# Optimization experiments

Hardware: AMD Instinct MI355X
Metric: run time of the kernel (lower is better)

Reference implementation:

```python
import jax, jax.numpy as jnp
import numpy as np

B, N, D, E, R, V = 8, 256, 64, 64, 32, 64
D_MIN, D_MAX = 0.0, 20.0


def _ln(x, g, b, eps=1e-5):
    m = jnp.mean(x, -1, keepdims=True)
    v = jnp.mean(jnp.square(x - m), -1, keepdims=True)
    return (x - m) * jax.lax.rsqrt(v + eps) * g + b


def setup_inputs() -> dict:
    key = jax.random.key(0)
    ks = jax.random.split(key, 12)
    w = lambda k, s: jax.random.normal(k, s, jnp.float32) * 0.02
    emb = w(ks[0], (V, D)).at[0].set(0.0)  # padding_idx=0 -> zero row
    return {
        "ligand_atom": jax.random.randint(ks[1], (B, N), 0, V),
        "ligand_pos": jax.random.normal(ks[2], (B, N, 3), jnp.float32),
        "edge_mask": jnp.ones((B, N, N), jnp.float32),
        "emb_table": emb,
        "ne_w": w(ks[3], (D, D)), "ne_b": jnp.zeros((D,), jnp.float32),
        "ne_g": jnp.ones((D,), jnp.float32), "ne_beta": jnp.zeros((D,), jnp.float32),
        "ee_w1": w(ks[4], (2 * D + R, E)), "ee_b1": jnp.zeros((E,), jnp.float32),
        "ee_w2": w(ks[5], (E, E)), "ee_b2": jnp.zeros((E,), jnp.float32),
        "ee_w3": w(ks[6], (E, E)), "ee_b3": jnp.zeros((E,), jnp.float32),
        "ee_g": jnp.ones((E,), jnp.float32), "ee_beta": jnp.zeros((E,), jnp.float32),
        "na_w1": w(ks[7], (D + E, D)), "na_b1": jnp.zeros((D,), jnp.float32),
        "na_w2": w(ks[8], (D, D)), "na_b2": jnp.zeros((D,), jnp.float32),
        "na_w3": w(ks[9], (D, D)), "na_b3": jnp.zeros((D,), jnp.float32),
        "na_g": jnp.ones((D,), jnp.float32), "na_beta": jnp.zeros((D,), jnp.float32),
    }


def reference(ligand_atom, ligand_pos, edge_mask, emb_table,
              ne_w, ne_b, ne_g, ne_beta,
              ee_w1, ee_b1, ee_w2, ee_b2, ee_w3, ee_b3, ee_g, ee_beta,
              na_w1, na_b1, na_w2, na_b2, na_w3, na_b3, na_g, na_beta):
    # node_embedder: Embedding -> ReLU -> Linear -> LayerNorm
    node = _ln(jax.nn.relu(emb_table[ligand_atom]) @ ne_w + ne_b, ne_g, ne_beta)  # [B,N,D]

    # pairwise distances, masked
    diff = ligand_pos[:, None, :, :] - ligand_pos[:, :, None, :]
    dist = jnp.sqrt(jnp.sum(diff * diff, -1) + 1e-10) * edge_mask  # [B,N,N]

    # RBF featurization
    mu = jnp.linspace(D_MIN, D_MAX, R)
    sigma = (D_MAX - D_MIN) / R
    rbf = jnp.exp(-jnp.square((dist[..., None] - mu) / sigma)) * edge_mask[..., None]  # [B,N,N,R]

    # edge_embedder: first Linear decomposed over [src | tar | rbf] slices (same math
    # as concat+Linear, avoids materializing the [B,N,N,2D+R] concat)
    Ws, Wt, Wr = ee_w1[:D], ee_w1[D:2 * D], ee_w1[2 * D:]
    # src[b,i,j]=node[b,j] (unsqueeze(1)), tar[b,i,j]=node[b,i] (unsqueeze(2))
    h = jax.nn.relu((node @ Ws)[:, None] + (node @ Wt)[:, :, None]
                    + jnp.einsum('bijr,re->bije', rbf, Wr) + ee_b1)
    h = jax.nn.relu(h @ ee_w2 + ee_b2)
    edge = _ln(h @ ee_w3 + ee_b3, ee_g, ee_beta)  # [B,N,N,E]

    # masked mean over dim=1, gated by (atom type clamped at 1)
    denom = jnp.sum(edge_mask[..., None], axis=1) + 1e-10  # [B,N,1]
    gate = jnp.minimum(ligand_atom, 1).astype(edge.dtype)[..., None]
    agg = jnp.sum(edge, axis=1) / denom * gate  # [B,N,E]

    x = jnp.concatenate([node, agg], -1)
    x = jax.nn.relu(x @ na_w1 + na_b1)
    x = jax.nn.relu(x @ na_w2 + na_b2)
    x = _ln(x @ na_w3 + na_b3, na_g, na_beta)
    return node + x, edge
```

## Files before the change

### kernel.cpp

```cpp
#include <hip/hip_runtime.h>
#include <math.h>

#define NB 8
#define NN 256
#define ND 64
#define NE 64
#define NR 32

typedef _Float16 half8 __attribute__((ext_vector_type(8)));
typedef _Float16 half4 __attribute__((ext_vector_type(4)));
typedef __fp16 fp16x2 __attribute__((ext_vector_type(2)));
typedef float f32x4 __attribute__((ext_vector_type(4)));
typedef int int4v __attribute__((ext_vector_type(4)));

__device__ __forceinline__ float rl(float x, int lane) {
    return __uint_as_float(__builtin_amdgcn_readlane(__float_as_uint(x), lane));
}

__device__ __forceinline__ float wave_sum64(float v) {
#pragma unroll
    for (int m = 32; m >= 1; m >>= 1) v += __shfl_xor(v, m, 64);
    return v;
}

__device__ __forceinline__ half4 mk4(float a, float b, float c, float d) {
    fp16x2 lo = __builtin_amdgcn_cvt_pkrtz(a, b);
    fp16x2 hi = __builtin_amdgcn_cvt_pkrtz(c, d);
    half4 r;
    r[0] = (_Float16)lo[0]; r[1] = (_Float16)lo[1];
    r[2] = (_Float16)hi[0]; r[3] = (_Float16)hi[1];
    return r;
}

__global__ __launch_bounds__(256) void k1_node(
    const int* __restrict__ atom, const float* __restrict__ emb,
    const float* __restrict__ ne_w, const float* __restrict__ ne_b,
    const float* __restrict__ ne_g, const float* __restrict__ ne_beta,
    const float* __restrict__ ee_w1, const float* __restrict__ ee_b1,
    const float* __restrict__ ee_w2, const float* __restrict__ ee_w3,
    float* __restrict__ ws_node, float* __restrict__ ws_s, float* __restrict__ ws_t,
    _Float16* __restrict__ wrT, _Float16* __restrict__ w2tH, _Float16* __restrict__ w3tH)
{
    if (blockIdx.x >= 512) {
        const int tid = (blockIdx.x - 512) * 256 + threadIdx.x;
        for (int idx = tid; idx < NE * NR; idx += 512) {
            const int e = idx >> 5, r = idx & 31;
            wrT[idx] = (_Float16)ee_w1[(2 * ND + r) * NE + e];
        }
        for (int idx = tid; idx < NE * NE; idx += 512) {
            const int n = idx >> 6, k = idx & 63;
            w2tH[idx] = (_Float16)ee_w2[k * NE + n];
            w3tH[idx] = (_Float16)ee_w3[k * NE + n];
        }
        return;
    }

    const int wave = threadIdx.x >> 6;
    const int lane = threadIdx.x & 63;
    const int row  = blockIdx.x * 4 + wave;

    const int a = atom[row];
    float ev = fmaxf(emb[a * ND + lane], 0.f);

    float a0 = 0.f, a1 = 0.f, a2 = 0.f, a3 = 0.f;
#pragma unroll
    for (int k = 0; k < ND; k += 4) {
        a0 = fmaf(rl(ev, k + 0), ne_w[(k + 0) * ND + lane], a0);
        a1 = fmaf(rl(ev, k + 1), ne_w[(k + 1) * ND + lane], a1);
        a2 = fmaf(rl(ev, k + 2), ne_w[(k + 2) * ND + lane], a2);
        a3 = fmaf(rl(ev, k + 3), ne_w[(k + 3) * ND + lane], a3);
    }
    float pre = ne_b[lane] + ((a0 + a1) + (a2 + a3));

    float mean = wave_sum64(pre) * (1.f / 64.f);
    float dv = pre - mean;
    float var = wave_sum64(dv * dv) * (1.f / 64.f);
    float nv = dv * rsqrtf(var + 1e-5f) * ne_g[lane] + ne_beta[lane];
    ws_node[row * ND + lane] = nv;

    float s0 = 0.f, s1 = 0.f, t0 = 0.f, t1 = 0.f;
#pragma unroll
    for (int k = 0; k < ND; k += 2) {
        const float n0 = rl(nv, k), n1 = rl(nv, k + 1);
        s0 = fmaf(n0, ee_w1[(k)     * NE + lane], s0);
        s1 = fmaf(n1, ee_w1[(k + 1) * NE + lane], s1);
        t0 = fmaf(n0, ee_w1[(ND + k)     * NE + lane], t0);
        t1 = fmaf(n1, ee_w1[(ND + k + 1) * NE + lane], t1);
    }
    ws_s[row * NE + lane] = ee_b1[lane] + s0 + s1;
    ws_t[row * NE + lane] = t0 + t1;
}

__global__ __launch_bounds__(256, 4) void k2_edge(
    const float* __restrict__ pos, const float* __restrict__ mask,
    const int* __restrict__ atom,
    const float* __restrict__ ws_s, const float* __restrict__ ws_t,
    const _Float16* __restrict__ wrT,
    const float* __restrict__ ee_b2, const float* __restrict__ ee_b3,
    const float* __restrict__ ee_g, const float* __restrict__ ee_beta,
    float* __restrict__ edge_out, float* __restrict__ ws_agg)
{
    __shared__ _Float16 wS[2048 + 4096 + 4096];
    __shared__ float sArr[64];
    __shared__ float b2Arr[64];
    __shared__ float aggp[4][64];
    __shared__ float mp[4];

    const int bj = blockIdx.x;
    const int b = bj >> 8, j = bj & 255;
    const int wave = threadIdx.x >> 6, lane = threadIdx.x & 63;
    const int quad = lane >> 4, col = lane & 15;
    const int ibase = wave * 64;

    {
        const int4v* src = (const int4v*)wrT;
        int4v* dst = (int4v*)wS;
        for (int k = threadIdx.x; k < 1280; k += 256) dst[k] = src[k];
        if (threadIdx.x < 64) {
            sArr[threadIdx.x]  = ws_s[bj * NE + threadIdx.x];
            b2Arr[threadIdx.x] = ee_b2[threadIdx.x];
        }
    }

    float b3v[4], gv[4], bev[4];
#pragma unroll
    for (int ot = 0; ot < 4; ot++) {
        const int e = ot * 16 + col;
        b3v[ot] = ee_b3[e];
        gv[ot]  = ee_g[e];
        bev[ot] = ee_beta[e];
    }
    const float pjx = pos[bj * 3 + 0], pjy = pos[bj * 3 + 1], pjz = pos[bj * 3 + 2];

    float murv[8];
#pragma unroll
    for (int t = 0; t < 8; t++) murv[t] = 1.0322580645f * (float)(quad * 8 + t);

    __syncthreads();
    const _Float16* wrS = wS;
    const _Float16* w2S = wS + 2048;
    const _Float16* w3S = wS + 2048 + 4096;

    float ag[4] = {0.f, 0.f, 0.f, 0.f};
    float msum = 0.f;

#pragma unroll 1
    for (int nt = 0; nt < 4; nt++) {
        const int i = ibase + nt * 16 + col;
        const int bi = b * NN + i;

        f32x4 tv[4];
#pragma unroll
        for (int mt = 0; mt < 4; mt++)
            tv[mt] = *(const f32x4*)(ws_t + bi * NE + mt * 16 + quad * 4);

        const float m = mask[bi * NN + j];
        const float dx = pjx - pos[bi * 3 + 0];
        const float dy = pjy - pos[bi * 3 + 1];
        const float dz = pjz - pos[bi * 3 + 2];
        const float dist = sqrtf(fmaf(dx, dx, fmaf(dy, dy, fmaf(dz, dz, 1e-10f)))) * m;
        msum += m;

        half8 rbfv;
#pragma unroll
        for (int t = 0; t < 8; t += 2) {
            const float u0 = fmaf(dist, 1.6f, -murv[t]);
            const float u1 = fmaf(dist, 1.6f, -murv[t + 1]);
            const float r0 = exp2f(u0 * u0 * (-1.44269504f)) * m;
            const float r1 = exp2f(u1 * u1 * (-1.44269504f)) * m;
            fp16x2 p = __builtin_amdgcn_cvt_pkrtz(r0, r1);
            rbfv[t] = (_Float16)p[0]; rbfv[t + 1] = (_Float16)p[1];
        }

        half4 b1f[4];
#pragma unroll
        for (int mt = 0; mt < 4; mt++) {
            half8 af = *(const half8*)(wrS + (mt * 16 + col) * NR + quad * 8);
            f32x4 z = {0.f, 0.f, 0.f, 0.f};
            f32x4 acc1 = __builtin_amdgcn_mfma_f32_16x16x32_f16(af, rbfv, z, 0, 0, 0);
            const f32x4 sv = *(const f32x4*)(sArr + mt * 16 + quad * 4);
            b1f[mt] = mk4(fmaxf(acc1[0] + tv[mt][0] + sv[0], 0.f),
                          fmaxf(acc1[1] + tv[mt][1] + sv[1], 0.f),
                          fmaxf(acc1[2] + tv[mt][2] + sv[2], 0.f),
                          fmaxf(acc1[3] + tv[mt][3] + sv[3], 0.f));
        }

        half4 a3f[4];
#pragma unroll
        for (int mt = 0; mt < 4; mt++) {
            f32x4 acc2 = {0.f, 0.f, 0.f, 0.f};
#pragma unroll
            for (int kt = 0; kt < 4; kt++) {
                half4 a2 = *(const half4*)(w2S + (mt * 16 + col) * NE + kt * 16 + quad * 4);
                acc2 = __builtin_amdgcn_mfma_f32_16x16x16f16(a2, b1f[kt], acc2, 0, 0, 0);
            }
            const f32x4 b2v = *(const f32x4*)(b2Arr + mt * 16 + quad * 4);
            a3f[mt] = mk4(fmaxf(acc2[0] + b2v[0], 0.f),
                          fmaxf(acc2[1] + b2v[1], 0.f),
                          fmaxf(acc2[2] + b2v[2], 0.f),
                          fmaxf(acc2[3] + b2v[3], 0.f));
        }

        f32x4 acc3[4];
#pragma unroll
        for (int ot = 0; ot < 4; ot++) {
            f32x4 acc = {0.f, 0.f, 0.f, 0.f};
#pragma unroll
            for (int kt = 0; kt < 4; kt++) {
                half4 b3f = *(const half4*)(w3S + (ot * 16 + col) * NE + kt * 16 + quad * 4);
                acc = __builtin_amdgcn_mfma_f32_16x16x16f16(a3f[kt], b3f, acc, 0, 0, 0);
            }
#pragma unroll
            for (int r = 0; r < 4; r++) acc[r] += b3v[ot];
            acc3[ot] = acc;
        }

#pragma unroll
        for (int r = 0; r < 4; r++) {
            float s = 0.f, q = 0.f;
#pragma unroll
            for (int ot = 0; ot < 4; ot++) {
                const float x = acc3[ot][r];
                s += x;
                q = fmaf(x, x, q);
            }
#pragma unroll
            for (int mm = 1; mm <= 8; mm <<= 1) {
                s += __shfl_xor(s, mm, 64);
                q += __shfl_xor(q, mm, 64);
            }
            const float mean = s * (1.f / 64.f);
            const float var = q * (1.f / 64.f) - mean * mean;
            const float rs = rsqrtf(var + 1e-5f);

            float* eb = edge_out +
                ((size_t)(b * NN + ibase + nt * 16 + quad * 4 + r) * NN + j) * NE + col;
#pragma unroll
            for (int ot = 0; ot < 4; ot++) {
                const float d = (acc3[ot][r] - mean) * rs;
                const float y = fmaf(d, gv[ot], bev[ot]);
                eb[ot * 16] = y;
                ag[ot] += y;
            }
        }
    }

#pragma unroll
    for (int ot = 0; ot < 4; ot++) {
        ag[ot] += __shfl_xor(ag[ot], 16, 64);
        ag[ot] += __shfl_xor(ag[ot], 32, 64);
    }
    if (quad == 0) {
#pragma unroll
        for (int ot = 0; ot < 4; ot++) aggp[wave][ot * 16 + col] = ag[ot];
    }
#pragma unroll
    for (int mm = 1; mm <= 8; mm <<= 1) msum += __shfl_xor(msum, mm, 64);
    if (lane == 0) mp[wave] = msum;

    __syncthreads();
    if (threadIdx.x < 64) {
        const int e = threadIdx.x;
        const float tot = aggp[0][e] + aggp[1][e] + aggp[2][e] + aggp[3][e];
        const float ms = mp[0] + mp[1] + mp[2] + mp[3];
        const float gate = (atom[bj] > 0) ? 1.f : 0.f;
        ws_agg[bj * NE + e] = tot / (ms + 1e-10f) * gate;
    }
}

__global__ __launch_bounds__(256) void k3_final(
    const float* __restrict__ ws_node, const float* __restrict__ ws_agg,
    const float* __restrict__ na_w1, const float* __restrict__ na_b1,
    const float* __restrict__ na_w2, const float* __restrict__ na_b2,
    const float* __restrict__ na_w3, const float* __restrict__ na_b3,
    const float* __restrict__ na_g, const float* __restrict__ na_beta,
    float* __restrict__ out0)
{
    const int wave = threadIdx.x >> 6;
    const int lane = threadIdx.x & 63;
    const int row = blockIdx.x * 4 + wave;

    const float nv = ws_node[row * ND + lane];
    const float av = ws_agg[row * ND + lane];

    float a0 = 0.f, a1 = 0.f, a2 = 0.f, a3 = 0.f;
#pragma unroll
    for (int k = 0; k < ND; k += 2) {
        a0 = fmaf(rl(nv, k),     na_w1[(k)     * ND + lane], a0);
        a1 = fmaf(rl(nv, k + 1), na_w1[(k + 1) * ND + lane], a1);
        a2 = fmaf(rl(av, k),     na_w1[(ND + k)     * ND + lane], a2);
        a3 = fmaf(rl(av, k + 1), na_w1[(ND + k + 1) * ND + lane], a3);
    }
    const float x1 = fmaxf(na_b1[lane] + (a0 + a1) + (a2 + a3), 0.f);

    float b0 = 0.f, b1 = 0.f, b2 = 0.f, b3 = 0.f;
#pragma unroll
    for (int k = 0; k < ND; k += 4) {
        b0 = fmaf(rl(x1, k + 0), na_w2[(k + 0) * ND + lane], b0);
        b1 = fmaf(rl(x1, k + 1), na_w2[(k + 1) * ND + lane], b1);
        b2 = fmaf(rl(x1, k + 2), na_w2[(k + 2) * ND + lane], b2);
        b3 = fmaf(rl(x1, k + 3), na_w2[(k + 3) * ND + lane], b3);
    }
    const float x2 = fmaxf(na_b2[lane] + (b0 + b1) + (b2 + b3), 0.f);

    float c0 = 0.f, c1 = 0.f, c2 = 0.f, c3 = 0.f;
#pragma unroll
    for (int k = 0; k < ND; k += 4) {
        c0 = fmaf(rl(x2, k + 0), na_w3[(k + 0) * ND + lane], c0);
        c1 = fmaf(rl(x2, k + 1), na_w3[(k + 1) * ND + lane], c1);
        c2 = fmaf(rl(x2, k + 2), na_w3[(k + 2) * ND + lane], c2);
        c3 = fmaf(rl(x2, k + 3), na_w3[(k + 3) * ND + lane], c3);
    }
    const float p3 = na_b3[lane] + (c0 + c1) + (c2 + c3);

    const float mean = wave_sum64(p3) * (1.f / 64.f);
    const float dvv = p3 - mean;
    const float var = wave_sum64(dvv * dvv) * (1.f / 64.f);
    const float x3 = dvv * rsqrtf(var + 1e-5f) * na_g[lane] + na_beta[lane];

    out0[row * ND + lane] = nv + x3;
}

extern "C" void kernel_launch(void* const* d_in, const int* in_sizes, int n_in,
                              void* d_out, int out_size, void* d_ws, size_t ws_size,
                              hipStream_t stream) {
    const int*   atom    = (const int*)d_in[0];
    const float* pos     = (const float*)d_in[1];
    const float* mask    = (const float*)d_in[2];
    const float* emb     = (const float*)d_in[3];
    const float* ne_w    = (const float*)d_in[4];
    const float* ne_b    = (const float*)d_in[5];
    const float* ne_g    = (const float*)d_in[6];
    const float* ne_beta = (const float*)d_in[7];
    const float* ee_w1   = (const float*)d_in[8];
    const float* ee_b1   = (const float*)d_in[9];
    const float* ee_w2   = (const float*)d_in[10];
    const float* ee_b2   = (const float*)d_in[11];
    const float* ee_w3   = (const float*)d_in[12];
    const float* ee_b3   = (const float*)d_in[13];
    const float* ee_g    = (const float*)d_in[14];
    const float* ee_beta = (const float*)d_in[15];
    const float* na_w1   = (const float*)d_in[16];
    const float* na_b1   = (const float*)d_in[17];
    const float* na_w2   = (const float*)d_in[18];
    const float* na_b2   = (const float*)d_in[19];
    const float* na_w3   = (const float*)d_in[20];
    const float* na_b3   = (const float*)d_in[21];
    const float* na_g    = (const float*)d_in[22];
    const float* na_beta = (const float*)d_in[23];

    float* out0     = (float*)d_out;
    float* edge_out = (float*)d_out + NB * NN * ND;

    float* ws_node = (float*)d_ws;
    float* ws_s    = ws_node + NB * NN * ND;
    float* ws_t    = ws_s + NB * NN * NE;
    float* ws_agg  = ws_t + NB * NN * NE;
    _Float16* wrT  = (_Float16*)(ws_agg + NB * NN * NE);
    _Float16* w2tH = wrT + NE * NR;
    _Float16* w3tH = w2tH + NE * NE;

    hipLaunchKernelGGL(k1_node, dim3(514), dim3(256), 0, stream,
                       atom, emb, ne_w, ne_b, ne_g, ne_beta, ee_w1, ee_b1,
                       ee_w2, ee_w3, ws_node, ws_s, ws_t, wrT, w2tH, w3tH);

    hipLaunchKernelGGL(k2_edge, dim3(NB * NN), dim3(256), 0, stream,
                       pos, mask, atom, ws_s, ws_t, wrT,
                       ee_b2, ee_b3, ee_g, ee_beta, edge_out, ws_agg);

    hipLaunchKernelGGL(k3_final, dim3(NB * NN / 4), dim3(256), 0, stream,
                       ws_node, ws_agg, na_w1, na_b1, na_w2, na_b2, na_w3, na_b3,
                       na_g, na_beta, out0);
}
```

Measured before the change: 308.9 us.

## Split edge kernel over four times more blocks and reduce aggregation with atomics

```diff
diff --git a/kernel.cpp b/kernel.cpp
--- a/kernel.cpp
+++ b/kernel.cpp
@@ -11,7 +11,6 @@
 typedef _Float16 half4 __attribute__((ext_vector_type(4)));
 typedef __fp16 fp16x2 __attribute__((ext_vector_type(2)));
 typedef float f32x4 __attribute__((ext_vector_type(4)));
-typedef int int4v __attribute__((ext_vector_type(4)));
 
 __device__ __forceinline__ float rl(float x, int lane) {
     return __uint_as_float(__builtin_amdgcn_readlane(__float_as_uint(x), lane));
@@ -93,35 +92,31 @@
 
 __global__ __launch_bounds__(256, 4) void k2_edge(
     const float* __restrict__ pos, const float* __restrict__ mask,
-    const int* __restrict__ atom,
     const float* __restrict__ ws_s, const float* __restrict__ ws_t,
-    const _Float16* __restrict__ wrT,
+    const _Float16* __restrict__ wrT, const _Float16* __restrict__ w2t,
+    const _Float16* __restrict__ w3t,
     const float* __restrict__ ee_b2, const float* __restrict__ ee_b3,
     const float* __restrict__ ee_g, const float* __restrict__ ee_beta,
-    float* __restrict__ edge_out, float* __restrict__ ws_agg)
+    float* __restrict__ edge_out, float* __restrict__ aggraw,
+    float* __restrict__ msumarr)
 {
-    __shared__ _Float16 wS[2048 + 4096 + 4096];
-    __shared__ float sArr[64];
-    __shared__ float b2Arr[64];
-    __shared__ float aggp[4][64];
-    __shared__ float mp[4];
-
-    const int bj = blockIdx.x;
+    const int blk = blockIdx.x;
+    const int iq = blk & 3;
+    const int bj = blk >> 2;
     const int b = bj >> 8, j = bj & 255;
     const int wave = threadIdx.x >> 6, lane = threadIdx.x & 63;
     const int quad = lane >> 4, col = lane & 15;
-    const int ibase = wave * 64;
-
-    {
-        const int4v* src = (const int4v*)wrT;
-        int4v* dst = (int4v*)wS;
-        for (int k = threadIdx.x; k < 1280; k += 256) dst[k] = src[k];
-        if (threadIdx.x < 64) {
-            sArr[threadIdx.x]  = ws_s[bj * NE + threadIdx.x];
-            b2Arr[threadIdx.x] = ee_b2[threadIdx.x];
-        }
-    }
-
+    const int itile = iq * 64 + wave * 16;
+    const int i = itile + col;
+    const int bi = b * NN + i;
+
+    f32x4 tv[4], sv[4], b2v[4];
+#pragma unroll
+    for (int mt = 0; mt < 4; mt++) {
+        tv[mt]  = *(const f32x4*)(ws_t + bi * NE + mt * 16 + quad * 4);
+        sv[mt]  = *(const f32x4*)(ws_s + bj * NE + mt * 16 + quad * 4);
+        b2v[mt] = *(const f32x4*)(ee_b2 + mt * 16 + quad * 4);
+    }
     float b3v[4], gv[4], bev[4];
 #pragma unroll
     for (int ot = 0; ot < 4; ot++) {
@@ -130,118 +125,95 @@
         gv[ot]  = ee_g[e];
         bev[ot] = ee_beta[e];
     }
+
     const float pjx = pos[bj * 3 + 0], pjy = pos[bj * 3 + 1], pjz = pos[bj * 3 + 2];
-
-    float murv[8];
-#pragma unroll
-    for (int t = 0; t < 8; t++) murv[t] = 1.0322580645f * (float)(quad * 8 + t);
-
-    __syncthreads();
-    const _Float16* wrS = wS;
-    const _Float16* w2S = wS + 2048;
-    const _Float16* w3S = wS + 2048 + 4096;
+    const float m = mask[bi * NN + j];
+    const float dx = pjx - pos[bi * 3 + 0];
+    const float dy = pjy - pos[bi * 3 + 1];
+    const float dz = pjz - pos[bi * 3 + 2];
+    const float dist = sqrtf(fmaf(dx, dx, fmaf(dy, dy, fmaf(dz, dz, 1e-10f)))) * m;
+
+    half8 rbfv;
+#pragma unroll
+    for (int t = 0; t < 8; t += 2) {
+        const float mu0 = 1.0322580645f * (float)(quad * 8 + t);
+        const float mu1 = 1.0322580645f * (float)(quad * 8 + t + 1);
+        const float u0 = fmaf(dist, 1.6f, -mu0);
+        const float u1 = fmaf(dist, 1.6f, -mu1);
+        const float r0 = exp2f(u0 * u0 * (-1.44269504f)) * m;
+        const float r1 = exp2f(u1 * u1 * (-1.44269504f)) * m;
+        fp16x2 p = __builtin_amdgcn_cvt_pkrtz(r0, r1);
+        rbfv[t] = (_Float16)p[0]; rbfv[t + 1] = (_Float16)p[1];
+    }
+
+    half4 b1f[4];
+#pragma unroll
+    for (int mt = 0; mt < 4; mt++) {
+        half8 af = *(const half8*)(wrT + (mt * 16 + col) * NR + quad * 8);
+        f32x4 z = {0.f, 0.f, 0.f, 0.f};
+        f32x4 acc1 = __builtin_amdgcn_mfma_f32_16x16x32_f16(af, rbfv, z, 0, 0, 0);
+        b1f[mt] = mk4(fmaxf(acc1[0] + tv[mt][0] + sv[mt][0], 0.f),
+                      fmaxf(acc1[1] + tv[mt][1] + sv[mt][1], 0.f),
+                      fmaxf(acc1[2] + tv[mt][2] + sv[mt][2], 0.f),
+                      fmaxf(acc1[3] + tv[mt][3] + sv[mt][3], 0.f));
+    }
+
+    half4 a3f[4];
+#pragma unroll
+    for (int mt = 0; mt < 4; mt++) {
+        f32x4 acc2 = {0.f, 0.f, 0.f, 0.f};
+#pragma unroll
+        for (int kt = 0; kt < 4; kt++) {
+            half4 a2 = *(const half4*)(w2t + (mt * 16 + col) * NE + kt * 16 + quad * 4);
+            acc2 = __builtin_amdgcn_mfma_f32_16x16x16f16(a2, b1f[kt], acc2, 0, 0, 0);
+        }
+        a3f[mt] = mk4(fmaxf(acc2[0] + b2v[mt][0], 0.f),
+                      fmaxf(acc2[1] + b2v[mt][1], 0.f),
+                      fmaxf(acc2[2] + b2v[mt][2], 0.f),
+                      fmaxf(acc2[3] + b2v[mt][3], 0.f));
+    }
+
+    f32x4 acc3[4];
+#pragma unroll
+    for (int ot = 0; ot < 4; ot++) {
+        f32x4 acc = {0.f, 0.f, 0.f, 0.f};
+#pragma unroll
+        for (int kt = 0; kt < 4; kt++) {
+            half4 b3f = *(const half4*)(w3t + (ot * 16 + col) * NE + kt * 16 + quad * 4);
+            acc = __builtin_amdgcn_mfma_f32_16x16x16f16(a3f[kt], b3f, acc, 0, 0, 0);
+        }
+#pragma unroll
+        for (int r = 0; r < 4; r++) acc[r] += b3v[ot];
+        acc3[ot] = acc;
+    }
 
     float ag[4] = {0.f, 0.f, 0.f, 0.f};
-    float msum = 0.f;
-
-#pragma unroll 1
-    for (int nt = 0; nt < 4; nt++) {
-        const int i = ibase + nt * 16 + col;
-        const int bi = b * NN + i;
-
-        f32x4 tv[4];
-#pragma unroll
-        for (int mt = 0; mt < 4; mt++)
-            tv[mt] = *(const f32x4*)(ws_t + bi * NE + mt * 16 + quad * 4);
-
-        const float m = mask[bi * NN + j];
-        const float dx = pjx - pos[bi * 3 + 0];
-        const float dy = pjy - pos[bi * 3 + 1];
-        const float dz = pjz - pos[bi * 3 + 2];
-        const float dist = sqrtf(fmaf(dx, dx, fmaf(dy, dy, fmaf(dz, dz, 1e-10f)))) * m;
-        msum += m;
-
-        half8 rbfv;
-#pragma unroll
-        for (int t = 0; t < 8; t += 2) {
-            const float u0 = fmaf(dist, 1.6f, -murv[t]);
-            const float u1 = fmaf(dist, 1.6f, -murv[t + 1]);
-            const float r0 = exp2f(u0 * u0 * (-1.44269504f)) * m;
-            const float r1 = exp2f(u1 * u1 * (-1.44269504f)) * m;
-            fp16x2 p = __builtin_amdgcn_cvt_pkrtz(r0, r1);
-            rbfv[t] = (_Float16)p[0]; rbfv[t + 1] = (_Float16)p[1];
-        }
-
-        half4 b1f[4];
-#pragma unroll
-        for (int mt = 0; mt < 4; mt++) {
-            half8 af = *(const half8*)(wrS + (mt * 16 + col) * NR + quad * 8);
-            f32x4 z = {0.f, 0.f, 0.f, 0.f};
-            f32x4 acc1 = __builtin_amdgcn_mfma_f32_16x16x32_f16(af, rbfv, z, 0, 0, 0);
-            const f32x4 sv = *(const f32x4*)(sArr + mt * 16 + quad * 4);
-            b1f[mt] = mk4(fmaxf(acc1[0] + tv[mt][0] + sv[0], 0.f),
-                          fmaxf(acc1[1] + tv[mt][1] + sv[1], 0.f),
-                          fmaxf(acc1[2] + tv[mt][2] + sv[2], 0.f),
-                          fmaxf(acc1[3] + tv[mt][3] + sv[3], 0.f));
-        }
-
-        half4 a3f[4];
-#pragma unroll
-        for (int mt = 0; mt < 4; mt++) {
-            f32x4 acc2 = {0.f, 0.f, 0.f, 0.f};
-#pragma unroll
-            for (int kt = 0; kt < 4; kt++) {
-                half4 a2 = *(const half4*)(w2S + (mt * 16 + col) * NE + kt * 16 + quad * 4);
-                acc2 = __builtin_amdgcn_mfma_f32_16x16x16f16(a2, b1f[kt], acc2, 0, 0, 0);
-            }
-            const f32x4 b2v = *(const f32x4*)(b2Arr + mt * 16 + quad * 4);
-            a3f[mt] = mk4(fmaxf(acc2[0] + b2v[0], 0.f),
-                          fmaxf(acc2[1] + b2v[1], 0.f),
-                          fmaxf(acc2[2] + b2v[2], 0.f),
-                          fmaxf(acc2[3] + b2v[3], 0.f));
-        }
-
-        f32x4 acc3[4];
+#pragma unroll
+    for (int r = 0; r < 4; r++) {
+        float s = 0.f, q = 0.f;
 #pragma unroll
         for (int ot = 0; ot < 4; ot++) {
-            f32x4 acc = {0.f, 0.f, 0.f, 0.f};
-#pragma unroll
-            for (int kt = 0; kt < 4; kt++) {
-                half4 b3f = *(const half4*)(w3S + (ot * 16 + col) * NE + kt * 16 + quad * 4);
-                acc = __builtin_amdgcn_mfma_f32_16x16x16f16(a3f[kt], b3f, acc, 0, 0, 0);
-            }
-#pragma unroll
-            for (int r = 0; r < 4; r++) acc[r] += b3v[ot];
-            acc3[ot] = acc;
-        }
-
-#pragma unroll
-        for (int r = 0; r < 4; r++) {
-            float s = 0.f, q = 0.f;
-#pragma unroll
-            for (int ot = 0; ot < 4; ot++) {
-                const float x = acc3[ot][r];
-                s += x;
-                q = fmaf(x, x, q);
-            }
-#pragma unroll
-            for (int mm = 1; mm <= 8; mm <<= 1) {
-                s += __shfl_xor(s, mm, 64);
-                q += __shfl_xor(q, mm, 64);
-            }
-            const float mean = s * (1.f / 64.f);
-            const float var = q * (1.f / 64.f) - mean * mean;
-            const float rs = rsqrtf(var + 1e-5f);
-
-            float* eb = edge_out +
-                ((size_t)(b * NN + ibase + nt * 16 + quad * 4 + r) * NN + j) * NE + col;
-#pragma unroll
-            for (int ot = 0; ot < 4; ot++) {
-                const float d = (acc3[ot][r] - mean) * rs;
-                const float y = fmaf(d, gv[ot], bev[ot]);
-                eb[ot * 16] = y;
-                ag[ot] += y;
-            }
+            const float x = acc3[ot][r];
+            s += x;
+            q = fmaf(x, x, q);
+        }
+#pragma unroll
+        for (int mm = 1; mm <= 8; mm <<= 1) {
+            s += __shfl_xor(s, mm, 64);
+            q += __shfl_xor(q, mm, 64);
+        }
+        const float mean = s * (1.f / 64.f);
+        const float var = q * (1.f / 64.f) - mean * mean;
+        const float rs = rsqrtf(var + 1e-5f);
+
+        float* eb = edge_out +
+            ((size_t)(b * NN + itile + quad * 4 + r) * NN + j) * NE + col;
+#pragma unroll
+        for (int ot = 0; ot < 4; ot++) {
+            const float d = (acc3[ot][r] - mean) * rs;
+            const float y = fmaf(d, gv[ot], bev[ot]);
+            eb[ot * 16] = y;
+            ag[ot] += y;
         }
     }
 
@@ -252,24 +224,19 @@
     }
     if (quad == 0) {
 #pragma unroll
-        for (int ot = 0; ot < 4; ot++) aggp[wave][ot * 16 + col] = ag[ot];
-    }
-#pragma unroll
-    for (int mm = 1; mm <= 8; mm <<= 1) msum += __shfl_xor(msum, mm, 64);
-    if (lane == 0) mp[wave] = msum;
-
-    __syncthreads();
-    if (threadIdx.x < 64) {
-        const int e = threadIdx.x;
-        const float tot = aggp[0][e] + aggp[1][e] + aggp[2][e] + aggp[3][e];
-        const float ms = mp[0] + mp[1] + mp[2] + mp[3];
-        const float gate = (atom[bj] > 0) ? 1.f : 0.f;
-        ws_agg[bj * NE + e] = tot / (ms + 1e-10f) * gate;
-    }
+        for (int ot = 0; ot < 4; ot++)
+            atomicAdd(&aggraw[bj * NE + ot * 16 + col], ag[ot]);
+    }
+    float ms = m;
+#pragma unroll
+    for (int mm = 1; mm <= 8; mm <<= 1) ms += __shfl_xor(ms, mm, 64);
+    if (lane == 0) atomicAdd(&msumarr[bj], ms);
 }
 
 __global__ __launch_bounds__(256) void k3_final(
-    const float* __restrict__ ws_node, const float* __restrict__ ws_agg,
+    const int* __restrict__ atom,
+    const float* __restrict__ ws_node, const float* __restrict__ aggraw,
+    const float* __restrict__ msumarr,
     const float* __restrict__ na_w1, const float* __restrict__ na_b1,
     const float* __restrict__ na_w2, const float* __restrict__ na_b2,
     const float* __restrict__ na_w3, const float* __restrict__ na_b3,
@@ -281,7 +248,8 @@
     const int row = blockIdx.x * 4 + wave;
 
     const float nv = ws_node[row * ND + lane];
-    const float av = ws_agg[row * ND + lane];
+    const float gate = (atom[row] > 0) ? 1.f : 0.f;
+    const float av = aggraw[row * NE + lane] / (msumarr[row] + 1e-10f) * gate;
 
     float a0 = 0.f, a1 = 0.f, a2 = 0.f, a3 = 0.f;
 #pragma unroll
@@ -355,20 +323,24 @@
     float* ws_node = (float*)d_ws;
     float* ws_s    = ws_node + NB * NN * ND;
     float* ws_t    = ws_s + NB * NN * NE;
-    float* ws_agg  = ws_t + NB * NN * NE;
-    _Float16* wrT  = (_Float16*)(ws_agg + NB * NN * NE);
+    float* aggraw  = ws_t + NB * NN * NE;
+    float* msumarr = aggraw + NB * NN * NE;
+    _Float16* wrT  = (_Float16*)(msumarr + NB * NN);
     _Float16* w2tH = wrT + NE * NR;
     _Float16* w3tH = w2tH + NE * NE;
+
+    hipMemsetAsync(aggraw, 0, (NB * NN * NE + NB * NN) * sizeof(float), stream);
 
     hipLaunchKernelGGL(k1_node, dim3(514), dim3(256), 0, stream,
                        atom, emb, ne_w, ne_b, ne_g, ne_beta, ee_w1, ee_b1,
                        ee_w2, ee_w3, ws_node, ws_s, ws_t, wrT, w2tH, w3tH);
 
-    hipLaunchKernelGGL(k2_edge, dim3(NB * NN), dim3(256), 0, stream,
-                       pos, mask, atom, ws_s, ws_t, wrT,
-                       ee_b2, ee_b3, ee_g, ee_beta, edge_out, ws_agg);
+    hipLaunchKernelGGL(k2_edge, dim3(NB * NN * 4), dim3(256), 0, stream,
+                       pos, mask, ws_s, ws_t, wrT, w2tH, w3tH,
+                       ee_b2, ee_b3, ee_g, ee_beta, edge_out, aggraw, msumarr);
 
     hipLaunchKernelGGL(k3_final, dim3(NB * NN / 4), dim3(256), 0, stream,
-                       ws_node, ws_agg, na_w1, na_b1, na_w2, na_b2, na_w3, na_b3,
+                       atom, ws_node, aggraw, msumarr,
+                       na_w1, na_b1, na_w2, na_b2, na_w3, na_b3,
                        na_g, na_beta, out0);
 }
```

Result: slower. 353.9 us (+14.6%).
